# Performance work log

Measured on AMD Instinct MI355X. Metric: run time of the kernel, lower is better.

Reference implementation:

```python
import jax, jax.numpy as jnp
import numpy as np

T, B, E, H, R = 1024, 8, 1024, 16, 16
HD = E // H


def setup_inputs() -> dict:
    key = jax.random.key(0)
    ks = jax.random.split(key, 10)
    w = lambda k, shape: (jax.random.normal(k, shape, jnp.float32) * 0.02)
    return {
        "query": jax.random.normal(ks[0], (T, B, E), jnp.float32),
        "in_proj_weight": w(ks[1], (3 * E, E)),
        "in_proj_bias": jnp.zeros((3 * E,), jnp.float32),
        "in_left": w(ks[2], (3 * E, R)),   # LrkLinear(rank -> 3E) weight
        "in_right": w(ks[3], (R, E)),      # LrkLinear(E -> rank) weight
        "out_proj_weight": w(ks[4], (E, E)),
        "out_proj_bias": jnp.zeros((E,), jnp.float32),
        "out_left": w(ks[5], (E, R)),
        "out_right": w(ks[6], (R, E)),
        "rel_pos_bias": w(ks[7], (H, T, T)),
    }


def reference(query, in_proj_weight, in_proj_bias, in_left, in_right,
              out_proj_weight, out_proj_bias, out_left, out_right, rel_pos_bias):
    t, b, e = query.shape
    hd = e // H
    scaling = float(hd) ** -0.5
    # fused in-projection: residual full-rank + low-rank branch
    acti = (jnp.einsum('tbe,fe->tbf', query, in_proj_weight) + in_proj_bias
            + jnp.einsum('tbr,fr->tbf', jnp.einsum('tbe,re->tbr', query, in_right), in_left))
    q, k, v = jnp.split(acti, 3, axis=-1)
    q = q * scaling
    # (T,B,E) -> (B,H,T,hd); matches torch view(T, B*H, hd).transpose(0,1)
    to_heads = lambda x: x.reshape(t, b, H, hd).transpose(1, 2, 0, 3)
    qh, kh, vh = to_heads(q), to_heads(k), to_heads(v)
    scores = jnp.einsum('bhtd,bhsd->bhts', qh, kh) + rel_pos_bias  # bias broadcasts over batch
    attn = jax.nn.softmax(scores, axis=-1)  # dropout_p = 0
    out = jnp.einsum('bhts,bhsd->bhtd', attn, vh)
    out = out.transpose(2, 0, 1, 3).reshape(t, b, e)
    # out-projection: residual full-rank + low-rank branch
    out = (jnp.einsum('tbe,fe->tbf', out, out_proj_weight) + out_proj_bias
           + jnp.einsum('tbr,fr->tbf', jnp.einsum('tbe,re->tbr', out, out_right), out_left))
    return out
```

## Files before the change

### kernel.cpp

```cpp
#include <hip/hip_runtime.h>
#include <hip/hip_bf16.h>


typedef __attribute__((ext_vector_type(8))) __bf16 bf16x8;
typedef __attribute__((ext_vector_type(4))) float f32x4;

__device__ __forceinline__ float bf2f(unsigned short u) {
  union { unsigned int i; float f; } v; v.i = ((unsigned int)u) << 16; return v.f;
}
__device__ __forceinline__ unsigned short f2bf(float f) {
  union { float f; unsigned int i; } v; v.f = f;
  unsigned int x = v.i;
  unsigned int r = x + 0x7FFFu + ((x >> 16) & 1u);
  return (unsigned short)(r >> 16);
}
__device__ __forceinline__ unsigned int pack2(float a, float b) {
  return (unsigned int)f2bf(a) | ((unsigned int)f2bf(b) << 16);
}
__device__ __forceinline__ float ld_in(const void* p, long idx, int isf32) {
  if (isf32) return ((const float*)p)[idx];
  return bf2f(((const unsigned short*)p)[idx]);
}
__device__ __forceinline__ void gl_lds16(const unsigned short* g, unsigned short* l) {
  __builtin_amdgcn_global_load_lds(
      (const __attribute__((address_space(1))) unsigned int*)g,
      (__attribute__((address_space(3))) unsigned int*)l, 16, 0, 0);
}

__global__ void detect_kernel(const unsigned int* __restrict__ q, int* __restrict__ flag) {
  __shared__ int cnt;
  if (threadIdx.x == 0) cnt = 0;
  __syncthreads();
  unsigned int w = q[threadIdx.x];
  int c = 0;
  if (((w >> 7) & 0xFFu) >= 0xC0u) c++;
  if (((w >> 23) & 0xFFu) >= 0xC0u) c++;
  atomicAdd(&cnt, c);
  __syncthreads();
  if (threadIdx.x == 0) flag[0] = (cnt >= 2) ? 1 : 0;
}

__global__ __launch_bounds__(256) void convert_bf16(
    const void* __restrict__ in, unsigned short* __restrict__ out,
    const int* __restrict__ flag) {
  long idx = ((long)blockIdx.x * 256 + threadIdx.x) * 8;
  if (flag[0]) {
    const float* p = (const float*)in + idx;
    float4 a = ((const float4*)p)[0], b = ((const float4*)p)[1];
    uint4 v;
    v.x = pack2(a.x, a.y); v.y = pack2(a.z, a.w);
    v.z = pack2(b.x, b.y); v.w = pack2(b.z, b.w);
    *(uint4*)(out + idx) = v;
  } else {
    *(uint4*)(out + idx) = *(const uint4*)((const unsigned short*)in + idx);
  }
}

__global__ __launch_bounds__(256) void eff_weights(
    const void* __restrict__ w, const void* __restrict__ left,
    const void* __restrict__ right, unsigned short* __restrict__ outw,
    const int* __restrict__ flag) {
  const int isf32 = flag[0];
  long idx = (long)blockIdx.x * 256 + threadIdx.x;
  long f = idx >> 10, e = idx & 1023;
  float acc = ld_in(w, idx, isf32);
#pragma unroll
  for (int r = 0; r < 16; ++r)
    acc += ld_in(left, (f << 4) + r, isf32) * ld_in(right, (r << 10) + e, isf32);
  outw[idx] = f2bf(acc);
}

__global__ __launch_bounds__(256) void inproj_kernel(
    const unsigned short* __restrict__ qbf,
    const unsigned short* __restrict__ weff,
    const void* __restrict__ bias,
    unsigned short* __restrict__ qh, unsigned short* __restrict__ kh,
    unsigned short* __restrict__ vt, const int* __restrict__ flag) {
  __shared__ __align__(16) unsigned short As[128 * 32];
  __shared__ __align__(16) unsigned short Bs[128 * 32];
  const int isf32 = flag[0];
  const int tid = threadIdx.x;
  const int wave = tid >> 6, lane = tid & 63, quad = lane >> 4, lrow = lane & 15;
  const int wr0 = (wave >> 1) * 64, wc0 = (wave & 1) * 64;
  const int fbase = blockIdx.x * 128, mbase = blockIdx.y * 128;
  const int srow = lane >> 2, scol = (lane & 3) * 8;
  const unsigned short* ag  = qbf  + (long)(mbase + 32 * wave + srow) * 1024 + scol;
  const unsigned short* ag2 = ag + 16 * 1024;
  const unsigned short* bg  = weff + (long)(fbase + 32 * wave + srow) * 1024 + scol;
  const unsigned short* bg2 = bg + 16 * 1024;
  unsigned short* la  = &As[(32 * wave) * 32];
  unsigned short* la2 = &As[(32 * wave + 16) * 32];
  unsigned short* lb  = &Bs[(32 * wave) * 32];
  unsigned short* lb2 = &Bs[(32 * wave + 16) * 32];

  f32x4 acc[4][4] = {};
  for (int k0 = 0; k0 < 1024; k0 += 32) {
    gl_lds16(ag + k0, la);
    gl_lds16(ag2 + k0, la2);
    gl_lds16(bg + k0, lb);
    gl_lds16(bg2 + k0, lb2);
    __syncthreads();
    bf16x8 af[4], bfv[4];
#pragma unroll
    for (int mi = 0; mi < 4; ++mi)
      af[mi] = *(const bf16x8*)&As[(wr0 + mi * 16 + lrow) * 32 + quad * 8];
#pragma unroll
    for (int ni = 0; ni < 4; ++ni)
      bfv[ni] = *(const bf16x8*)&Bs[(wc0 + ni * 16 + lrow) * 32 + quad * 8];
#pragma unroll
    for (int mi = 0; mi < 4; ++mi)
#pragma unroll
      for (int ni = 0; ni < 4; ++ni)
        acc[mi][ni] = __builtin_amdgcn_mfma_f32_16x16x32_bf16(af[mi], bfv[ni], acc[mi][ni], 0, 0, 0);
    __syncthreads();
  }
  const int which = fbase >> 10;
  const int h = ((fbase + wc0) >> 6) & 15;
#pragma unroll
  for (int ni = 0; ni < 4; ++ni) {
    const int d = ni * 16 + lrow;
    const float bv = ld_in(bias, fbase + wc0 + d, isf32);
#pragma unroll
    for (int mi = 0; mi < 4; ++mi)
#pragma unroll
      for (int r = 0; r < 4; ++r) {
        const int m = mbase + wr0 + mi * 16 + quad * 4 + r;
        const int t = m >> 3, b = m & 7;
        const float val = acc[mi][ni][r] + bv;
        if (which == 0)
          qh[((long)(b * 16 + h) * 1024 + t) * 64 + d] = f2bf(val * 0.125f);
        else if (which == 1)
          kh[((long)(b * 16 + h) * 1024 + t) * 64 + d] = f2bf(val);
        else
          vt[((long)(b * 16 + h) * 64 + d) * 1024 + t] = f2bf(val);
      }
  }
}

__global__ __launch_bounds__(256) void attn_kernel(
    const unsigned short* __restrict__ qh, const unsigned short* __restrict__ kh,
    const unsigned short* __restrict__ vt, const void* __restrict__ rpb,
    const unsigned short* __restrict__ pre,
    unsigned short* __restrict__ ctx, const int* __restrict__ flag) {
  __shared__ __align__(16) unsigned short Ks[2][4096];
  __shared__ __align__(16) unsigned short Vs[2][4096];
  __shared__ __align__(16) unsigned short Ps[4][1024];
  const int isf32 = flag[0];
  const int tid = threadIdx.x;
  const int wave = tid >> 6, lane = tid & 63, quad = lane >> 4, lrow = lane & 15;
  const int b = blockIdx.y & 7, h = blockIdx.y >> 3, bh = b * 16 + h;
  const int t0 = blockIdx.x * 64;

  const unsigned short* qbase = qh + ((long)(bh * 1024) + t0 + wave * 16 + lrow) * 64;
  bf16x8 qf0 = *(const bf16x8*)(qbase + quad * 8);
  bf16x8 qf1 = *(const bf16x8*)(qbase + 32 + quad * 8);

  const unsigned short* kbase = kh + (long)bh * 65536;
  const unsigned short* vbase = vt + (long)bh * 65536;

  const long bidx0 = ((long)h * 1024 + t0 + wave * 16 + quad * 4) * 1024 + lrow;
  const unsigned short* bs16 = pre ? pre : (const unsigned short*)rpb;
  const bool bf32 = (isf32 && pre == nullptr);
  const float* bsf = (const float*)rpb;

  const int j0 = 2 * wave, j1 = j0 + 1;
  const int kk0 = j0 >> 2, ii0 = j0 & 3, kk1 = j1 >> 2, ii1 = j1 & 3;
  const int sr = lane >> 2, sc = (lane & 3) * 8;
  const unsigned short* kg0 = kbase + (long)(16 * ii0 + sr) * 64 + kk0 * 32 + sc;
  const unsigned short* kg1 = kbase + (long)(16 * ii1 + sr) * 64 + kk1 * 32 + sc;
  const unsigned short* vg0 = vbase + (long)(16 * ii0 + sr) * 1024 + kk0 * 32 + sc;
  const unsigned short* vg1 = vbase + (long)(16 * ii1 + sr) * 1024 + kk1 * 32 + sc;
  const int lo0 = kk0 * 2048 + ii0 * 512, lo1 = kk1 * 2048 + ii1 * 512;

  f32x4 oacc[4] = {};
  float rsum[4] = {0.f, 0.f, 0.f, 0.f};
  unsigned int bcur[4][4], bnxt[4][4];

  gl_lds16(kg0, &Ks[0][lo0]);
  gl_lds16(kg1, &Ks[0][lo1]);
  gl_lds16(vg0, &Vs[0][lo0]);
  gl_lds16(vg1, &Vs[0][lo1]);
  if (bf32) {
#pragma unroll
    for (int r = 0; r < 4; ++r)
#pragma unroll
      for (int n = 0; n < 4; ++n)
        bcur[r][n] = __float_as_uint(bsf[bidx0 + r * 1024 + n * 16]);
  } else {
#pragma unroll
    for (int r = 0; r < 4; ++r)
#pragma unroll
      for (int n = 0; n < 4; ++n)
        bcur[r][n] = (unsigned int)bs16[bidx0 + r * 1024 + n * 16];
  }
  __syncthreads();

  for (int t = 0; t < 16; ++t) {
    const int cur = t & 1;
    const int s0 = t << 6;
    if (t < 15) {
      const int sn = s0 + 64;
      gl_lds16(kg0 + (long)sn * 64, &Ks[cur ^ 1][lo0]);
      gl_lds16(kg1 + (long)sn * 64, &Ks[cur ^ 1][lo1]);
      gl_lds16(vg0 + sn, &Vs[cur ^ 1][lo0]);
      gl_lds16(vg1 + sn, &Vs[cur ^ 1][lo1]);
      if (bf32) {
#pragma unroll
        for (int r = 0; r < 4; ++r)
#pragma unroll
          for (int n = 0; n < 4; ++n)
            bnxt[r][n] = __float_as_uint(bsf[bidx0 + r * 1024 + sn + n * 16]);
      } else {
#pragma unroll
        for (int r = 0; r < 4; ++r)
#pragma unroll
          for (int n = 0; n < 4; ++n)
            bnxt[r][n] = (unsigned int)bs16[bidx0 + r * 1024 + sn + n * 16];
      }
    }

    f32x4 sacc[4] = {};
#pragma unroll
    for (int n = 0; n < 4; ++n) {
      bf16x8 kf0 = *(const bf16x8*)&Ks[cur][(n * 16 + lrow) * 32 + quad * 8];
      bf16x8 kf1 = *(const bf16x8*)&Ks[cur][2048 + (n * 16 + lrow) * 32 + quad * 8];
      sacc[n] = __builtin_amdgcn_mfma_f32_16x16x32_bf16(qf0, kf0, sacc[n], 0, 0, 0);
      sacc[n] = __builtin_amdgcn_mfma_f32_16x16x32_bf16(qf1, kf1, sacc[n], 0, 0, 0);
    }

#pragma unroll
    for (int n = 0; n < 4; ++n)
#pragma unroll
      for (int r = 0; r < 4; ++r) {
        const int row = quad * 4 + r;
        const float bv = bf32 ? __uint_as_float(bcur[r][n])
                              : bf2f((unsigned short)bcur[r][n]);
        const float p = __expf(sacc[n][r] + bv);
        rsum[r] += p;
        Ps[wave][(row * 64 + n * 16 + lrow) ^ ((row & 7) << 3)] = f2bf(p);
      }

    asm volatile("s_waitcnt lgkmcnt(0)" ::: "memory");

#pragma unroll
    for (int kk = 0; kk < 2; ++kk) {
      bf16x8 pf = *(const bf16x8*)&Ps[wave][(lrow * 64 + kk * 32 + quad * 8) ^ ((lrow & 7) << 3)];
#pragma unroll
      for (int n = 0; n < 4; ++n) {
        bf16x8 vf = *(const bf16x8*)&Vs[cur][kk * 2048 + (n * 16 + lrow) * 32 + quad * 8];
        oacc[n] = __builtin_amdgcn_mfma_f32_16x16x32_bf16(pf, vf, oacc[n], 0, 0, 0);
      }
    }
    __syncthreads();
    if (t < 15) {
#pragma unroll
      for (int r = 0; r < 4; ++r)
#pragma unroll
        for (int n = 0; n < 4; ++n) bcur[r][n] = bnxt[r][n];
    }
  }

#pragma unroll
  for (int msk = 1; msk <= 8; msk <<= 1)
#pragma unroll
    for (int r = 0; r < 4; ++r)
      rsum[r] += __shfl_xor(rsum[r], msk, 64);

  float linv[4];
#pragma unroll
  for (int r = 0; r < 4; ++r) linv[r] = 1.0f / rsum[r];
#pragma unroll
  for (int n = 0; n < 4; ++n)
#pragma unroll
    for (int r = 0; r < 4; ++r) {
      const int t = t0 + wave * 16 + quad * 4 + r;
      ctx[((long)t * 8 + b) * 1024 + h * 64 + n * 16 + lrow] = f2bf(oacc[n][r] * linv[r]);
    }
}

__global__ __launch_bounds__(256) void outproj_kernel(
    const unsigned short* __restrict__ ctx, const unsigned short* __restrict__ weff,
    const void* __restrict__ bias, void* __restrict__ out,
    const int* __restrict__ flag) {
  __shared__ __align__(16) unsigned short As[128 * 32];
  __shared__ __align__(16) unsigned short Bs[128 * 32];
  const int isf32 = flag[0];
  const int tid = threadIdx.x;
  const int wave = tid >> 6, lane = tid & 63, quad = lane >> 4, lrow = lane & 15;
  const int wr0 = (wave >> 1) * 64, wc0 = (wave & 1) * 64;
  const int fbase = blockIdx.x * 128, mbase = blockIdx.y * 128;
  const int srow = lane >> 2, scol = (lane & 3) * 8;
  const unsigned short* ag  = ctx  + (long)(mbase + 32 * wave + srow) * 1024 + scol;
  const unsigned short* ag2 = ag + 16 * 1024;
  const unsigned short* bg  = weff + (long)(fbase + 32 * wave + srow) * 1024 + scol;
  const unsigned short* bg2 = bg + 16 * 1024;
  unsigned short* la  = &As[(32 * wave) * 32];
  unsigned short* la2 = &As[(32 * wave + 16) * 32];
  unsigned short* lb  = &Bs[(32 * wave) * 32];
  unsigned short* lb2 = &Bs[(32 * wave + 16) * 32];

  f32x4 acc[4][4] = {};
  for (int k0 = 0; k0 < 1024; k0 += 32) {
    gl_lds16(ag + k0, la);
    gl_lds16(ag2 + k0, la2);
    gl_lds16(bg + k0, lb);
    gl_lds16(bg2 + k0, lb2);
    __syncthreads();
    bf16x8 af[4], bfv[4];
#pragma unroll
    for (int mi = 0; mi < 4; ++mi)
      af[mi] = *(const bf16x8*)&As[(wr0 + mi * 16 + lrow) * 32 + quad * 8];
#pragma unroll
    for (int ni = 0; ni < 4; ++ni)
      bfv[ni] = *(const bf16x8*)&Bs[(wc0 + ni * 16 + lrow) * 32 + quad * 8];
#pragma unroll
    for (int mi = 0; mi < 4; ++mi)
#pragma unroll
      for (int ni = 0; ni < 4; ++ni)
        acc[mi][ni] = __builtin_amdgcn_mfma_f32_16x16x32_bf16(af[mi], bfv[ni], acc[mi][ni], 0, 0, 0);
    __syncthreads();
  }
#pragma unroll
  for (int ni = 0; ni < 4; ++ni) {
    const int f = fbase + wc0 + ni * 16 + lrow;
    const float bv = ld_in(bias, f, isf32);
#pragma unroll
    for (int mi = 0; mi < 4; ++mi)
#pragma unroll
      for (int r = 0; r < 4; ++r) {
        const int m = mbase + wr0 + mi * 16 + quad * 4 + r;
        const float val = acc[mi][ni][r] + bv;
        if (isf32) ((float*)out)[(long)m * 1024 + f] = val;
        else       ((unsigned short*)out)[(long)m * 1024 + f] = f2bf(val);
      }
  }
}

extern "C" void kernel_launch(void* const* d_in, const int* in_sizes, int n_in,
                              void* d_out, int out_size, void* d_ws, size_t ws_size,
                              hipStream_t stream) {
  (void)out_size;
  static const int EXP[10] = {8388608, 3145728, 3072, 49152, 16384,
                              1048576, 1024, 16384, 16384, 16777216};
  if (n_in != 10) return;
  for (int i = 0; i < 10; ++i) if (in_sizes[i] != EXP[i]) return;

  const void* query = d_in[0];
  const void* ipw = d_in[1];  const void* ipb = d_in[2];
  const void* il  = d_in[3];  const void* ir  = d_in[4];
  const void* opw = d_in[5];  const void* opb = d_in[6];
  const void* ol  = d_in[7];  const void* orr = d_in[8];
  const void* rpb = d_in[9];

  int* flag = (int*)d_ws;
  unsigned short* base = (unsigned short*)d_ws + 16;
  unsigned short* w_in_eff  = base;
  unsigned short* w_out_eff = w_in_eff + (long)3072 * 1024;
  unsigned short* qh  = w_out_eff + (long)1024 * 1024;
  unsigned short* kh  = qh + 8388608L;
  unsigned short* vt  = kh + 8388608L;
  unsigned short* ctx = vt + 8388608L;
  unsigned short* rpbbf = ctx + 8388608L;
  unsigned short* qbf = ctx;
  const size_t NEED_FULL = 32 + (3145728L + 1048576L + 4L * 8388608L + 16777216L) * 2;
  const bool big = ws_size >= NEED_FULL;

  detect_kernel<<<dim3(1), dim3(64), 0, stream>>>((const unsigned int*)query, flag);
  if (big)
    convert_bf16<<<dim3(8192), dim3(256), 0, stream>>>(rpb, rpbbf, flag);
  convert_bf16<<<dim3(4096), dim3(256), 0, stream>>>(query, qbf, flag);
  eff_weights<<<dim3(12288), dim3(256), 0, stream>>>(ipw, il, ir, w_in_eff, flag);
  eff_weights<<<dim3(4096), dim3(256), 0, stream>>>(opw, ol, orr, w_out_eff, flag);
  inproj_kernel<<<dim3(24, 64), dim3(256), 0, stream>>>(qbf, w_in_eff, ipb, qh, kh, vt, flag);
  attn_kernel<<<dim3(16, 128), dim3(256), 0, stream>>>(qh, kh, vt, rpb,
                                                       big ? rpbbf : nullptr, ctx, flag);
  outproj_kernel<<<dim3(8, 64), dim3(256), 0, stream>>>(ctx, w_out_eff, opb, d_out, flag);
}
```

Before: 432.4 us.

## Double-buffer LDS tiles in in-projection and out-projection GEMM kernels

Both projection GEMM kernels now keep two LDS buffers per operand. The global-to-LDS loads for the next K tile are issued before the MFMAs on the current tile, so memory latency overlaps with matrix math instead of sitting behind a barrier each iteration. This doubles the LDS footprint per block, which may lower occupancy, and it relies on the trailing barrier to drain the asynchronous loads before the next iteration reads them.

```diff
diff --git a/kernel.cpp b/kernel.cpp
--- a/kernel.cpp
+++ b/kernel.cpp
@@ -76,8 +76,8 @@
     const void* __restrict__ bias,
     unsigned short* __restrict__ qh, unsigned short* __restrict__ kh,
     unsigned short* __restrict__ vt, const int* __restrict__ flag) {
-  __shared__ __align__(16) unsigned short As[128 * 32];
-  __shared__ __align__(16) unsigned short Bs[128 * 32];
+  __shared__ __align__(16) unsigned short As[2][128 * 32];
+  __shared__ __align__(16) unsigned short Bs[2][128 * 32];
   const int isf32 = flag[0];
   const int tid = threadIdx.x;
   const int wave = tid >> 6, lane = tid & 63, quad = lane >> 4, lrow = lane & 15;
@@ -88,25 +88,32 @@
   const unsigned short* ag2 = ag + 16 * 1024;
   const unsigned short* bg  = weff + (long)(fbase + 32 * wave + srow) * 1024 + scol;
   const unsigned short* bg2 = bg + 16 * 1024;
-  unsigned short* la  = &As[(32 * wave) * 32];
-  unsigned short* la2 = &As[(32 * wave + 16) * 32];
-  unsigned short* lb  = &Bs[(32 * wave) * 32];
-  unsigned short* lb2 = &Bs[(32 * wave + 16) * 32];
+  const int lof  = (32 * wave) * 32;
+  const int lof2 = (32 * wave + 16) * 32;
 
   f32x4 acc[4][4] = {};
-  for (int k0 = 0; k0 < 1024; k0 += 32) {
-    gl_lds16(ag + k0, la);
-    gl_lds16(ag2 + k0, la2);
-    gl_lds16(bg + k0, lb);
-    gl_lds16(bg2 + k0, lb2);
-    __syncthreads();
+  gl_lds16(ag, &As[0][lof]);
+  gl_lds16(ag2, &As[0][lof2]);
+  gl_lds16(bg, &Bs[0][lof]);
+  gl_lds16(bg2, &Bs[0][lof2]);
+  __syncthreads();
+
+  for (int it = 0; it < 32; ++it) {
+    const int cur = it & 1;
+    if (it < 31) {
+      const int kn = (it + 1) * 32;
+      gl_lds16(ag + kn, &As[cur ^ 1][lof]);
+      gl_lds16(ag2 + kn, &As[cur ^ 1][lof2]);
+      gl_lds16(bg + kn, &Bs[cur ^ 1][lof]);
+      gl_lds16(bg2 + kn, &Bs[cur ^ 1][lof2]);
+    }
     bf16x8 af[4], bfv[4];
 #pragma unroll
     for (int mi = 0; mi < 4; ++mi)
-      af[mi] = *(const bf16x8*)&As[(wr0 + mi * 16 + lrow) * 32 + quad * 8];
+      af[mi] = *(const bf16x8*)&As[cur][(wr0 + mi * 16 + lrow) * 32 + quad * 8];
 #pragma unroll
     for (int ni = 0; ni < 4; ++ni)
-      bfv[ni] = *(const bf16x8*)&Bs[(wc0 + ni * 16 + lrow) * 32 + quad * 8];
+      bfv[ni] = *(const bf16x8*)&Bs[cur][(wc0 + ni * 16 + lrow) * 32 + quad * 8];
 #pragma unroll
     for (int mi = 0; mi < 4; ++mi)
 #pragma unroll
@@ -282,8 +289,8 @@
     const unsigned short* __restrict__ ctx, const unsigned short* __restrict__ weff,
     const void* __restrict__ bias, void* __restrict__ out,
     const int* __restrict__ flag) {
-  __shared__ __align__(16) unsigned short As[128 * 32];
-  __shared__ __align__(16) unsigned short Bs[128 * 32];
+  __shared__ __align__(16) unsigned short As[2][128 * 32];
+  __shared__ __align__(16) unsigned short Bs[2][128 * 32];
   const int isf32 = flag[0];
   const int tid = threadIdx.x;
   const int wave = tid >> 6, lane = tid & 63, quad = lane >> 4, lrow = lane & 15;
@@ -294,25 +301,32 @@
   const unsigned short* ag2 = ag + 16 * 1024;
   const unsigned short* bg  = weff + (long)(fbase + 32 * wave + srow) * 1024 + scol;
   const unsigned short* bg2 = bg + 16 * 1024;
-  unsigned short* la  = &As[(32 * wave) * 32];
-  unsigned short* la2 = &As[(32 * wave + 16) * 32];
-  unsigned short* lb  = &Bs[(32 * wave) * 32];
-  unsigned short* lb2 = &Bs[(32 * wave + 16) * 32];
+  const int lof  = (32 * wave) * 32;
+  const int lof2 = (32 * wave + 16) * 32;
 
   f32x4 acc[4][4] = {};
-  for (int k0 = 0; k0 < 1024; k0 += 32) {
-    gl_lds16(ag + k0, la);
-    gl_lds16(ag2 + k0, la2);
-    gl_lds16(bg + k0, lb);
-    gl_lds16(bg2 + k0, lb2);
-    __syncthreads();
+  gl_lds16(ag, &As[0][lof]);
+  gl_lds16(ag2, &As[0][lof2]);
+  gl_lds16(bg, &Bs[0][lof]);
+  gl_lds16(bg2, &Bs[0][lof2]);
+  __syncthreads();
+
+  for (int it = 0; it < 32; ++it) {
+    const int cur = it & 1;
+    if (it < 31) {
+      const int kn = (it + 1) * 32;
+      gl_lds16(ag + kn, &As[cur ^ 1][lof]);
+      gl_lds16(ag2 + kn, &As[cur ^ 1][lof2]);
+      gl_lds16(bg + kn, &Bs[cur ^ 1][lof]);
+      gl_lds16(bg2 + kn, &Bs[cur ^ 1][lof2]);
+    }
     bf16x8 af[4], bfv[4];
 #pragma unroll
     for (int mi = 0; mi < 4; ++mi)
-      af[mi] = *(const bf16x8*)&As[(wr0 + mi * 16 + lrow) * 32 + quad * 8];
+      af[mi] = *(const bf16x8*)&As[cur][(wr0 + mi * 16 + lrow) * 32 + quad * 8];
 #pragma unroll
     for (int ni = 0; ni < 4; ++ni)
-      bfv[ni] = *(const bf16x8*)&Bs[(wc0 + ni * 16 + lrow) * 32 + quad * 8];
+      bfv[ni] = *(const bf16x8*)&Bs[cur][(wc0 + ni * 16 + lrow) * 32 + quad * 8];
 #pragma unroll
     for (int mi = 0; mi < 4; ++mi)
 #pragma unroll
```

New measurement: 440.7 us. Within noise of the previous version (+1.9%).
